# Performance work log

Measured on AMD Instinct MI355X. Metric: run time of the kernel, lower is better.

The kernel has to match this reference:

```python
import jax, jax.numpy as jnp
import numpy as np

NUM_HEADS = 8


def setup_inputs() -> dict:
    key = jax.random.key(0)
    k0, k1, k2 = jax.random.split(key, 3)
    B, C, D, H, W = 2, 256, 16, 16, 8
    x = jax.random.normal(k0, (B, C, D, H, W), dtype=jnp.float32)
    # 1x1x1 Conv3d weights are pointwise linear maps over channels
    w_qkv = jax.random.normal(k1, (3 * C, C), dtype=jnp.float32) * 0.02
    b_qkv = jnp.zeros((3 * C,), dtype=jnp.float32)
    w_out = jax.random.normal(k2, (C, C), dtype=jnp.float32) * 0.02
    b_out = jnp.zeros((C,), dtype=jnp.float32)
    return {"x": x, "w_qkv": w_qkv, "b_qkv": b_qkv, "w_out": w_out, "b_out": b_out}


def reference(x, w_qkv, b_qkv, w_out, b_out):
    b, c, d, h, w = x.shape
    nh = NUM_HEADS
    hd = c // nh
    scale = hd ** (-0.5)
    n = d * h * w
    xf = x.reshape(b, c, n)  # flatten spatial volume to N tokens
    # to_qkv: pointwise conv == channel-mixing matmul
    qkv = jnp.einsum('oc,bcn->bon', w_qkv, xf) + b_qkv[None, :, None]
    # torch: view(b, H, 3*hd, N) then chunk(3, dim=2) -> per-head channel grouping
    qkv = qkv.reshape(b, nh, 3 * hd, n)
    q, k, v = jnp.split(qkv, 3, axis=2)  # each (b, nh, hd, n)
    sim = jnp.einsum('bhcn,bhcm->bhnm', q, k) * scale  # (b, nh, N, N)
    attn = jax.nn.softmax(sim, axis=-1)
    out = jnp.einsum('bhnm,bhcm->bhcn', attn, v)  # (b, nh, hd, N)
    out = out.reshape(b, c, n)
    out = jnp.einsum('oc,bcn->bon', w_out, out) + b_out[None, :, None]
    return x + out.reshape(b, c, d, h, w)
```

## Files before the change

### kernel.cpp

```cpp
#include <hip/hip_runtime.h>
#include <hip/hip_bf16.h>
#include <math.h>

#define BB 2
#define CC 256
#define NH 8
#define HD 32
#define NN 2048
#define KSPAN 1024
#define QBLK 64
#define KTILE 128
#define QK_SCALE 0.25500917f

typedef __attribute__((ext_vector_type(8))) short short8;
typedef __attribute__((ext_vector_type(8))) unsigned short ushort8;
typedef __attribute__((ext_vector_type(4))) float f32x4;

__device__ inline unsigned short f2bf(float f) {
    __hip_bfloat16 h = __float2bfloat16(f);
    return __builtin_bit_cast(unsigned short, h);
}
__device__ inline float bf2f(unsigned short s) {
    unsigned u = (unsigned)s << 16;
    return __builtin_bit_cast(float, u);
}
__device__ inline int kperm(int k) {
    return 32 * (k >> 5) + 16 * ((k >> 2) & 1) + 4 * ((k >> 3) & 3) + (k & 3);
}

__global__ __launch_bounds__(256) void prep(const float* __restrict__ x,
                                            const float* __restrict__ wq,
                                            const float* __restrict__ wo,
                                            unsigned short* __restrict__ xt,
                                            unsigned short* __restrict__ wqb,
                                            unsigned short* __restrict__ wob) {
    const int blk = blockIdx.x, t = threadIdx.x;
    if (blk < 256) {
        const int b = blk >> 7, tile = blk & 127;
        const int c0 = (tile >> 5) * 64, n0 = (tile & 31) * 64;
        __shared__ unsigned short Ts[64][72];
        const float* xb = x + ((size_t)b * CC + c0) * NN + n0;
        const int cl = t >> 4, nl = (t & 15) * 4;
#pragma unroll
        for (int i = 0; i < 4; ++i) {
            float4 v = *(const float4*)&xb[(size_t)(cl + 16 * i) * NN + nl];
            Ts[nl + 0][cl + 16 * i] = f2bf(v.x);
            Ts[nl + 1][cl + 16 * i] = f2bf(v.y);
            Ts[nl + 2][cl + 16 * i] = f2bf(v.z);
            Ts[nl + 3][cl + 16 * i] = f2bf(v.w);
        }
        __syncthreads();
        const int nr = t >> 2, cb = (t & 3) * 16;
        unsigned short* dst = xt + ((size_t)b * NN + n0 + nr) * CC + c0 + cb;
        *(ushort8*)&dst[0] = *(const ushort8*)&Ts[nr][cb];
        *(ushort8*)&dst[8] = *(const ushort8*)&Ts[nr][cb + 8];
    } else if (blk < 264) {
        const int base = (blk - 256) * 24576 + t * 4;
#pragma unroll
        for (int i = 0; i < 24; ++i) {
            int idx = base + i * 1024;
            float4 v = *(const float4*)&wq[idx];
            ushort4 r;
            r.x = f2bf(v.x); r.y = f2bf(v.y); r.z = f2bf(v.z); r.w = f2bf(v.w);
            *(ushort4*)&wqb[idx] = r;
        }
    } else {
        const int base = (blk - 264) * 32768 + t * 4;
#pragma unroll
        for (int i = 0; i < 32; ++i) {
            int idx = base + i * 1024;
            float4 v = *(const float4*)&wo[idx];
            ushort4 r;
            r.x = f2bf(v.x); r.y = f2bf(v.y); r.z = f2bf(v.z); r.w = f2bf(v.w);
            *(ushort4*)&wob[idx] = r;
        }
    }
}

__global__ __launch_bounds__(256) void qkv_mfma(const unsigned short* __restrict__ xt,
                                                const unsigned short* __restrict__ wqb,
                                                const float* __restrict__ bias,
                                                unsigned short* __restrict__ qt,
                                                unsigned short* __restrict__ ktt,
                                                unsigned short* __restrict__ vt) {
    const int b = blockIdx.z, m0 = blockIdx.y * 64, n0 = blockIdx.x * 64;
    const int t = threadIdx.x, lane = t & 63, wid = t >> 6;
    const int g = lane >> 4, ln = lane & 15;
    __shared__ __align__(16) unsigned short Aw[4][64][36];
    __shared__ __align__(16) unsigned short Bx[4][64][36];
    f32x4 acc[4] = {};
    const unsigned short* xb = xt + ((size_t)b * NN + n0) * CC;

    const int sm = t & 63, sch = t >> 6;
    for (int kh = 0; kh < 2; ++kh) {
        __syncthreads();
#pragma unroll
        for (int j = 0; j < 4; ++j) {
            *(ushort8*)&Aw[sch][sm][j * 8] =
                *(const ushort8*)&wqb[(size_t)(m0 + sm) * CC + kh * 128 + sch * 32 + j * 8];
            *(ushort8*)&Bx[sch][sm][j * 8] =
                *(const ushort8*)&xb[(size_t)sm * CC + kh * 128 + sch * 32 + j * 8];
        }
        __syncthreads();
#pragma unroll
        for (int ks = 0; ks < 4; ++ks) {
            short8 aW = *(const short8*)&Aw[ks][wid * 16 + ln][g * 8];
#pragma unroll
            for (int nt = 0; nt < 4; ++nt) {
                short8 bX = *(const short8*)&Bx[ks][nt * 16 + ln][g * 8];
                acc[nt] = __builtin_amdgcn_mfma_f32_16x16x32_bf16(aW, bX, acc[nt], 0, 0, 0);
            }
        }
    }
    const int obase = m0 + wid * 16 + 4 * g;
    const int sect = obase % 96;
    const int type = sect >> 5;
    const int head = obase / 96;
    const int cb4 = obase & 31;
    float bv[4];
#pragma unroll
    for (int r = 0; r < 4; ++r) bv[r] = bias[obase + r];
    if (type == 2) {
#pragma unroll
        for (int nt = 0; nt < 4; ++nt) {
            int n = n0 + nt * 16 + ln;
#pragma unroll
            for (int r = 0; r < 4; ++r)
                vt[((size_t)(b * NH + head) * HD + cb4 + r) * NN + n] = f2bf(acc[nt][r] + bv[r]);
        }
    } else {
        const float sc = (type == 0) ? QK_SCALE : 1.0f;
        unsigned short* dst = (type == 0) ? qt : ktt;
#pragma unroll
        for (int nt = 0; nt < 4; ++nt) {
            int n = n0 + nt * 16 + ln;
            ushort4 r4;
            r4.x = f2bf((acc[nt][0] + bv[0]) * sc);
            r4.y = f2bf((acc[nt][1] + bv[1]) * sc);
            r4.z = f2bf((acc[nt][2] + bv[2]) * sc);
            r4.w = f2bf((acc[nt][3] + bv[3]) * sc);
            *(ushort4*)&dst[((size_t)(b * NH + head) * NN + n) * HD + cb4] = r4;
        }
    }
}

__global__ __launch_bounds__(512) void attn_mfma(const unsigned short* __restrict__ Qt,
                                                 const unsigned short* __restrict__ Kt,
                                                 const unsigned short* __restrict__ Vt,
                                                 unsigned short* __restrict__ aout_t) {
    const int b = blockIdx.z, h = blockIdx.y;
    const int n0 = blockIdx.x * QBLK;
    const int t = threadIdx.x;
    const int lane = t & 63, wid = t >> 6;
    const int g = lane >> 4, ln = lane & 15;
    const int qg = wid & 3, whalf = wid >> 2;

    __shared__ __align__(16) unsigned short Qs[QBLK][40];
    __shared__ __align__(16) unsigned short Ks[2][KTILE][40];
    __shared__ __align__(16) unsigned short Vs[2][HD][136];

    const unsigned short* qb = Qt + ((size_t)(b * NH + h) * NN + n0) * HD;
    const unsigned short* kb = Kt + (size_t)(b * NH + h) * NN * HD;
    const unsigned short* vb = Vt + (size_t)(b * NH + h) * HD * NN;

    if (t < 256) {
        int q = t >> 2, ch = (t & 3) * 8;
        *(ushort8*)&Qs[q][ch] = *(const ushort8*)&qb[(size_t)q * HD + ch];
    }
    __syncthreads();
    const short8 bQ = *(const short8*)&Qs[qg * 16 + ln][g * 8];

    const int th = t & 255, sthalf = t >> 8;
    const int sk = th >> 2, sch = (th & 3) * 8;
    const int row0 = kperm(sk), row1 = kperm(sk + 64);
    const int vcc = th >> 3, vn = (th & 7) * 16;
    const size_t hbase = (size_t)sthalf * KSPAN;

    ushort8 kpre0, kpre1, vpre0, vpre1;
    {
        const unsigned short* ksrc = kb + (hbase + sk) * HD + sch;
        kpre0 = *(const ushort8*)ksrc;
        kpre1 = *(const ushort8*)(ksrc + (size_t)64 * HD);
        const unsigned short* vsrc = vb + (size_t)vcc * NN + hbase + vn;
        vpre0 = *(const ushort8*)vsrc;
        vpre1 = *(const ushort8*)(vsrc + 8);
    }

    float m_run = -1e30f, l_run = 0.f;
    f32x4 oacc[2];
    const f32x4 zero4 = {0.f, 0.f, 0.f, 0.f};
    oacc[0] = zero4; oacc[1] = zero4;

    for (int kt = 0; kt < KSPAN; kt += KTILE) {
        __syncthreads();
        *(ushort8*)&Ks[sthalf][row0][sch] = kpre0;
        *(ushort8*)&Ks[sthalf][row1][sch] = kpre1;
        *(ushort8*)&Vs[sthalf][vcc][vn]     = vpre0;
        *(ushort8*)&Vs[sthalf][vcc][vn + 8] = vpre1;
        __syncthreads();
        if (kt + KTILE < KSPAN) {
            const unsigned short* ksrc = kb + (hbase + kt + KTILE + sk) * HD + sch;
            kpre0 = *(const ushort8*)ksrc;
            kpre1 = *(const ushort8*)(ksrc + (size_t)64 * HD);
            const unsigned short* vsrc = vb + (size_t)vcc * NN + hbase + kt + KTILE + vn;
            vpre0 = *(const ushort8*)vsrc;
            vpre1 = *(const ushort8*)(vsrc + 8);
        }

        f32x4 sacc[8];
        __builtin_amdgcn_s_setprio(1);
#pragma unroll
        for (int t8 = 0; t8 < 8; ++t8) {
            short8 aK = *(const short8*)&Ks[whalf][t8 * 16 + ln][g * 8];
            sacc[t8] = __builtin_amdgcn_mfma_f32_16x16x32_bf16(aK, bQ, zero4, 0, 0, 0);
        }
        __builtin_amdgcn_s_setprio(0);

        float mx[8];
#pragma unroll
        for (int t8 = 0; t8 < 8; ++t8)
            mx[t8] = fmaxf(fmaxf(sacc[t8][0], sacc[t8][1]), fmaxf(sacc[t8][2], sacc[t8][3]));
        float tmax = fmaxf(fmaxf(fmaxf(mx[0], mx[1]), fmaxf(mx[2], mx[3])),
                           fmaxf(fmaxf(mx[4], mx[5]), fmaxf(mx[6], mx[7])));
        tmax = fmaxf(tmax, __shfl_xor(tmax, 16));
        tmax = fmaxf(tmax, __shfl_xor(tmax, 32));
        float mnew = fmaxf(m_run, tmax);
        float rsc = exp2f(m_run - mnew);
#pragma unroll
        for (int t8 = 0; t8 < 8; ++t8) {
            sacc[t8][0] = exp2f(sacc[t8][0] - mnew);
            sacc[t8][1] = exp2f(sacc[t8][1] - mnew);
            sacc[t8][2] = exp2f(sacc[t8][2] - mnew);
            sacc[t8][3] = exp2f(sacc[t8][3] - mnew);
        }
        float ps[8];
#pragma unroll
        for (int t8 = 0; t8 < 8; ++t8)
            ps[t8] = (sacc[t8][0] + sacc[t8][1]) + (sacc[t8][2] + sacc[t8][3]);
        float lsum = ((ps[0] + ps[1]) + (ps[2] + ps[3])) + ((ps[4] + ps[5]) + (ps[6] + ps[7]));
        lsum += __shfl_xor(lsum, 16);
        lsum += __shfl_xor(lsum, 32);
        l_run = l_run * rsc + lsum;
        m_run = mnew;

#pragma unroll
        for (int r = 0; r < 4; ++r) {
            float rr = __shfl(rsc, 4 * g + r);
            oacc[0][r] *= rr;
            oacc[1][r] *= rr;
        }

        short8 aP[4];
#pragma unroll
        for (int kc = 0; kc < 4; ++kc) {
#pragma unroll
            for (int u = 0; u < 2; ++u) {
#pragma unroll
                for (int r = 0; r < 4; ++r)
                    aP[kc][u * 4 + r] = (short)f2bf(sacc[2 * kc + u][r]);
            }
        }

        __builtin_amdgcn_s_setprio(1);
#pragma unroll
        for (int kc = 0; kc < 4; ++kc) {
            short8 bV0 = *(const short8*)&Vs[whalf][ln][kc * 32 + g * 8];
            short8 bV1 = *(const short8*)&Vs[whalf][16 + ln][kc * 32 + g * 8];
            oacc[0] = __builtin_amdgcn_mfma_f32_16x16x32_bf16(aP[kc], bV0, oacc[0], 0, 0, 0);
            oacc[1] = __builtin_amdgcn_mfma_f32_16x16x32_bf16(aP[kc], bV1, oacc[1], 0, 0, 0);
        }
        __builtin_amdgcn_s_setprio(0);
    }

    __syncthreads();
    float*  Of  = (float*)&Ks[0][0][0];
    float2* MLs = (float2*)&Vs[0][0][0];
#pragma unroll
    for (int ct = 0; ct < 2; ++ct)
#pragma unroll
        for (int r = 0; r < 4; ++r)
            Of[((whalf * 64) + qg * 16 + 4 * g + r) * 40 + ct * 16 + ln] = oacc[ct][r];
    if (g == 0) MLs[whalf * 64 + qg * 16 + ln] = make_float2(m_run, l_run);
    __syncthreads();
    {
        const int q = t >> 3, c0 = (t & 7) * 4;
        f32x4 o0 = *(const f32x4*)&Of[(size_t)q * 40 + c0];
        f32x4 o1 = *(const f32x4*)&Of[(size_t)(64 + q) * 40 + c0];
        float2 ml0 = MLs[q], ml1 = MLs[64 + q];
        float M = fmaxf(ml0.x, ml1.x);
        float w0 = exp2f(ml0.x - M), w1 = exp2f(ml1.x - M);
        float dinv = 1.0f / (w0 * ml0.y + w1 * ml1.y);
        w0 *= dinv; w1 *= dinv;
        ushort4 r4;
        r4.x = f2bf(w0 * o0[0] + w1 * o1[0]);
        r4.y = f2bf(w0 * o0[1] + w1 * o1[1]);
        r4.z = f2bf(w0 * o0[2] + w1 * o1[2]);
        r4.w = f2bf(w0 * o0[3] + w1 * o1[3]);
        *(ushort4*)&aout_t[((size_t)b * NN + n0 + q) * CC + h * HD + c0] = r4;
    }
}

__global__ __launch_bounds__(256) void proj_mfma(const unsigned short* __restrict__ aout_t,
                                                 const unsigned short* __restrict__ wob,
                                                 const float* __restrict__ bias,
                                                 const float* __restrict__ x,
                                                 float* __restrict__ out) {
    const int b = blockIdx.z, m0 = blockIdx.y * 64, n0 = blockIdx.x * 32;
    const int t = threadIdx.x, lane = t & 63, wid = t >> 6;
    const int g = lane >> 4, ln = lane & 15;
    __shared__ __align__(16) unsigned short Aw[4][64][36];
    __shared__ __align__(16) unsigned short Bx[4][32][36];
    f32x4 acc[2] = {};
    const unsigned short* ab = aout_t + ((size_t)b * NN + n0) * CC;

    const int sm = t & 63, sch = t >> 6;
    const int bn = t & 31, bch = t >> 5;
    for (int kh = 0; kh < 2; ++kh) {
        __syncthreads();
#pragma unroll
        for (int j = 0; j < 4; ++j)
            *(ushort8*)&Aw[sch][sm][j * 8] =
                *(const ushort8*)&wob[(size_t)(m0 + sm) * CC + kh * 128 + sch * 32 + j * 8];
        {
            int ks = bch >> 1, off = (bch & 1) * 16;
            const unsigned short* src = &ab[(size_t)bn * CC + kh * 128 + ks * 32 + off];
            *(ushort8*)&Bx[ks][bn][off]     = *(const ushort8*)&src[0];
            *(ushort8*)&Bx[ks][bn][off + 8] = *(const ushort8*)&src[8];
        }
        __syncthreads();
#pragma unroll
        for (int ks = 0; ks < 4; ++ks) {
            short8 aW = *(const short8*)&Aw[ks][wid * 16 + ln][g * 8];
#pragma unroll
            for (int nt = 0; nt < 2; ++nt) {
                short8 bX = *(const short8*)&Bx[ks][nt * 16 + ln][g * 8];
                acc[nt] = __builtin_amdgcn_mfma_f32_16x16x32_bf16(aW, bX, acc[nt], 0, 0, 0);
            }
        }
    }
    const int mbase = m0 + wid * 16 + 4 * g;
    float bv[4];
#pragma unroll
    for (int r = 0; r < 4; ++r) bv[r] = bias[mbase + r];
#pragma unroll
    for (int nt = 0; nt < 2; ++nt) {
        int n = n0 + nt * 16 + ln;
#pragma unroll
        for (int r = 0; r < 4; ++r) {
            size_t off = ((size_t)b * CC + mbase + r) * NN + n;
            out[off] = acc[nt][r] + bv[r] + x[off];
        }
    }
}

extern "C" void kernel_launch(void* const* d_in, const int* in_sizes, int n_in,
                              void* d_out, int out_size, void* d_ws, size_t ws_size,
                              hipStream_t stream) {
    const float* x     = (const float*)d_in[0];
    const float* w_qkv = (const float*)d_in[1];
    const float* b_qkv = (const float*)d_in[2];
    const float* w_out = (const float*)d_in[3];
    const float* b_out = (const float*)d_in[4];
    float* out = (float*)d_out;

    unsigned short* xt     = (unsigned short*)d_ws;
    unsigned short* wqb    = xt  + (size_t)BB * NN * CC;
    unsigned short* wob    = wqb + (size_t)768 * CC;
    unsigned short* qt     = wob + (size_t)CC * CC;
    unsigned short* ktt    = qt  + (size_t)BB * NH * NN * HD;
    unsigned short* vt     = ktt + (size_t)BB * NH * NN * HD;
    unsigned short* aout_t = vt  + (size_t)BB * NH * NN * HD;

    prep<<<dim3(266), 256, 0, stream>>>(x, w_qkv, w_out, xt, wqb, wob);
    qkv_mfma<<<dim3(NN / 64, 768 / 64, BB), 256, 0, stream>>>(xt, wqb, b_qkv, qt, ktt, vt);
    attn_mfma<<<dim3(NN / QBLK, NH, BB), 512, 0, stream>>>(qt, ktt, vt, aout_t);
    proj_mfma<<<dim3(NN / 32, CC / 64, BB), 256, 0, stream>>>(aout_t, wob, b_out, x, out);
}
```

Measured before the change: 54.65 us.

## Fuse bf16 conversion into GEMMs and restructure attention with lazy rescale

Removes the separate prep kernel. The QKV and output-projection kernels now load fp32 x and weights directly and convert them to bf16 while staging into shared memory, which saves one launch and a round trip through the workspace. The attention kernel moves to 64-key tiles with double-buffered K/V shared memory and one barrier per iteration. It also skips the online-softmax rescale unless the running max rises by more than a threshold. In exchange, every GEMM block redundantly converts the weights, and the lazy rescale lets exp values grow up to 2^8 before being renormalised.

```diff
diff --git a/kernel.cpp b/kernel.cpp
--- a/kernel.cpp
+++ b/kernel.cpp
@@ -9,7 +9,8 @@
 #define NN 2048
 #define KSPAN 1024
 #define QBLK 64
-#define KTILE 128
+#define KTILE 64
+#define NITER (KSPAN / KTILE)
 #define QK_SCALE 0.25500917f
 
 typedef __attribute__((ext_vector_type(8))) short short8;
@@ -20,65 +21,12 @@
     __hip_bfloat16 h = __float2bfloat16(f);
     return __builtin_bit_cast(unsigned short, h);
 }
-__device__ inline float bf2f(unsigned short s) {
-    unsigned u = (unsigned)s << 16;
-    return __builtin_bit_cast(float, u);
-}
 __device__ inline int kperm(int k) {
     return 32 * (k >> 5) + 16 * ((k >> 2) & 1) + 4 * ((k >> 3) & 3) + (k & 3);
 }
 
-__global__ __launch_bounds__(256) void prep(const float* __restrict__ x,
-                                            const float* __restrict__ wq,
-                                            const float* __restrict__ wo,
-                                            unsigned short* __restrict__ xt,
-                                            unsigned short* __restrict__ wqb,
-                                            unsigned short* __restrict__ wob) {
-    const int blk = blockIdx.x, t = threadIdx.x;
-    if (blk < 256) {
-        const int b = blk >> 7, tile = blk & 127;
-        const int c0 = (tile >> 5) * 64, n0 = (tile & 31) * 64;
-        __shared__ unsigned short Ts[64][72];
-        const float* xb = x + ((size_t)b * CC + c0) * NN + n0;
-        const int cl = t >> 4, nl = (t & 15) * 4;
-#pragma unroll
-        for (int i = 0; i < 4; ++i) {
-            float4 v = *(const float4*)&xb[(size_t)(cl + 16 * i) * NN + nl];
-            Ts[nl + 0][cl + 16 * i] = f2bf(v.x);
-            Ts[nl + 1][cl + 16 * i] = f2bf(v.y);
-            Ts[nl + 2][cl + 16 * i] = f2bf(v.z);
-            Ts[nl + 3][cl + 16 * i] = f2bf(v.w);
-        }
-        __syncthreads();
-        const int nr = t >> 2, cb = (t & 3) * 16;
-        unsigned short* dst = xt + ((size_t)b * NN + n0 + nr) * CC + c0 + cb;
-        *(ushort8*)&dst[0] = *(const ushort8*)&Ts[nr][cb];
-        *(ushort8*)&dst[8] = *(const ushort8*)&Ts[nr][cb + 8];
-    } else if (blk < 264) {
-        const int base = (blk - 256) * 24576 + t * 4;
-#pragma unroll
-        for (int i = 0; i < 24; ++i) {
-            int idx = base + i * 1024;
-            float4 v = *(const float4*)&wq[idx];
-            ushort4 r;
-            r.x = f2bf(v.x); r.y = f2bf(v.y); r.z = f2bf(v.z); r.w = f2bf(v.w);
-            *(ushort4*)&wqb[idx] = r;
-        }
-    } else {
-        const int base = (blk - 264) * 32768 + t * 4;
-#pragma unroll
-        for (int i = 0; i < 32; ++i) {
-            int idx = base + i * 1024;
-            float4 v = *(const float4*)&wo[idx];
-            ushort4 r;
-            r.x = f2bf(v.x); r.y = f2bf(v.y); r.z = f2bf(v.z); r.w = f2bf(v.w);
-            *(ushort4*)&wob[idx] = r;
-        }
-    }
-}
-
-__global__ __launch_bounds__(256) void qkv_mfma(const unsigned short* __restrict__ xt,
-                                                const unsigned short* __restrict__ wqb,
+__global__ __launch_bounds__(256) void qkv_mfma(const float* __restrict__ x,
+                                                const float* __restrict__ wq,
                                                 const float* __restrict__ bias,
                                                 unsigned short* __restrict__ qt,
                                                 unsigned short* __restrict__ ktt,
@@ -89,17 +37,39 @@
     __shared__ __align__(16) unsigned short Aw[4][64][36];
     __shared__ __align__(16) unsigned short Bx[4][64][36];
     f32x4 acc[4] = {};
-    const unsigned short* xb = xt + ((size_t)b * NN + n0) * CC;
 
     const int sm = t & 63, sch = t >> 6;
+    const int pc = t >> 4, pn = t & 15;
+    const int c0 = pc * 8, nl = pn * 4;
+    const float* xb = x + (size_t)b * CC * NN + n0;
+
     for (int kh = 0; kh < 2; ++kh) {
         __syncthreads();
-#pragma unroll
-        for (int j = 0; j < 4; ++j) {
-            *(ushort8*)&Aw[sch][sm][j * 8] =
-                *(const ushort8*)&wqb[(size_t)(m0 + sm) * CC + kh * 128 + sch * 32 + j * 8];
-            *(ushort8*)&Bx[sch][sm][j * 8] =
-                *(const ushort8*)&xb[(size_t)sm * CC + kh * 128 + sch * 32 + j * 8];
+        {
+            const float* wsrc = wq + (size_t)(m0 + sm) * CC + kh * 128 + sch * 32;
+            float wv[32];
+#pragma unroll
+            for (int j = 0; j < 8; ++j) *(float4*)&wv[j * 4] = *(const float4*)&wsrc[j * 4];
+#pragma unroll
+            for (int j2 = 0; j2 < 4; ++j2) {
+                ushort8 p;
+#pragma unroll
+                for (int e = 0; e < 8; ++e) p[e] = f2bf(wv[j2 * 8 + e]);
+                *(ushort8*)&Aw[sch][sm][j2 * 8] = p;
+            }
+        }
+        {
+            const float* xsrc = xb + (size_t)(kh * 128 + c0) * NN + nl;
+            float xv[8][4];
+#pragma unroll
+            for (int i = 0; i < 8; ++i) *(float4*)&xv[i][0] = *(const float4*)&xsrc[(size_t)i * NN];
+#pragma unroll
+            for (int i2 = 0; i2 < 4; ++i2) {
+                ushort8 p;
+#pragma unroll
+                for (int e = 0; e < 8; ++e) p[e] = f2bf(xv[e][i2]);
+                *(ushort8*)&Bx[pc >> 2][nl + i2][(pc & 3) * 8] = p;
+            }
         }
         __syncthreads();
 #pragma unroll
@@ -156,8 +126,8 @@
     const int qg = wid & 3, whalf = wid >> 2;
 
     __shared__ __align__(16) unsigned short Qs[QBLK][40];
-    __shared__ __align__(16) unsigned short Ks[2][KTILE][40];
-    __shared__ __align__(16) unsigned short Vs[2][HD][136];
+    __shared__ __align__(16) unsigned short Ks[2][2][KTILE][40];
+    __shared__ __align__(16) unsigned short Vs[2][2][HD][72];
 
     const unsigned short* qb = Qt + ((size_t)(b * NH + h) * NN + n0) * HD;
     const unsigned short* kb = Kt + (size_t)(b * NH + h) * NN * HD;
@@ -172,100 +142,88 @@
 
     const int th = t & 255, sthalf = t >> 8;
     const int sk = th >> 2, sch = (th & 3) * 8;
-    const int row0 = kperm(sk), row1 = kperm(sk + 64);
-    const int vcc = th >> 3, vn = (th & 7) * 16;
+    const int rowK = kperm(sk);
+    const int vcc = th >> 3, vn = (th & 7) * 8;
     const size_t hbase = (size_t)sthalf * KSPAN;
 
-    ushort8 kpre0, kpre1, vpre0, vpre1;
-    {
-        const unsigned short* ksrc = kb + (hbase + sk) * HD + sch;
-        kpre0 = *(const ushort8*)ksrc;
-        kpre1 = *(const ushort8*)(ksrc + (size_t)64 * HD);
-        const unsigned short* vsrc = vb + (size_t)vcc * NN + hbase + vn;
-        vpre0 = *(const ushort8*)vsrc;
-        vpre1 = *(const ushort8*)(vsrc + 8);
-    }
+    ushort8 kpre, vpre;
+    kpre = *(const ushort8*)&kb[(hbase + sk) * HD + sch];
+    vpre = *(const ushort8*)&vb[(size_t)vcc * NN + hbase + vn];
 
     float m_run = -1e30f, l_run = 0.f;
     f32x4 oacc[2];
     const f32x4 zero4 = {0.f, 0.f, 0.f, 0.f};
     oacc[0] = zero4; oacc[1] = zero4;
 
-    for (int kt = 0; kt < KSPAN; kt += KTILE) {
-        __syncthreads();
-        *(ushort8*)&Ks[sthalf][row0][sch] = kpre0;
-        *(ushort8*)&Ks[sthalf][row1][sch] = kpre1;
-        *(ushort8*)&Vs[sthalf][vcc][vn]     = vpre0;
-        *(ushort8*)&Vs[sthalf][vcc][vn + 8] = vpre1;
-        __syncthreads();
-        if (kt + KTILE < KSPAN) {
-            const unsigned short* ksrc = kb + (hbase + kt + KTILE + sk) * HD + sch;
-            kpre0 = *(const ushort8*)ksrc;
-            kpre1 = *(const ushort8*)(ksrc + (size_t)64 * HD);
-            const unsigned short* vsrc = vb + (size_t)vcc * NN + hbase + kt + KTILE + vn;
-            vpre0 = *(const ushort8*)vsrc;
-            vpre1 = *(const ushort8*)(vsrc + 8);
-        }
-
-        f32x4 sacc[8];
+    for (int it = 0; it < NITER; ++it) {
+        const int buf = it & 1;
+        *(ushort8*)&Ks[sthalf][buf][rowK][sch] = kpre;
+        *(ushort8*)&Vs[sthalf][buf][vcc][vn]   = vpre;
+        if (it + 1 < NITER) {
+            size_t kt = hbase + (size_t)(it + 1) * KTILE;
+            kpre = *(const ushort8*)&kb[(kt + sk) * HD + sch];
+            vpre = *(const ushort8*)&vb[(size_t)vcc * NN + kt + vn];
+        }
+        __syncthreads();
+
+        f32x4 sacc[4];
         __builtin_amdgcn_s_setprio(1);
 #pragma unroll
-        for (int t8 = 0; t8 < 8; ++t8) {
-            short8 aK = *(const short8*)&Ks[whalf][t8 * 16 + ln][g * 8];
+        for (int t8 = 0; t8 < 4; ++t8) {
+            short8 aK = *(const short8*)&Ks[whalf][buf][t8 * 16 + ln][g * 8];
             sacc[t8] = __builtin_amdgcn_mfma_f32_16x16x32_bf16(aK, bQ, zero4, 0, 0, 0);
         }
         __builtin_amdgcn_s_setprio(0);
 
-        float mx[8];
-#pragma unroll
-        for (int t8 = 0; t8 < 8; ++t8)
+        float mx[4];
+#pragma unroll
+        for (int t8 = 0; t8 < 4; ++t8)
             mx[t8] = fmaxf(fmaxf(sacc[t8][0], sacc[t8][1]), fmaxf(sacc[t8][2], sacc[t8][3]));
-        float tmax = fmaxf(fmaxf(fmaxf(mx[0], mx[1]), fmaxf(mx[2], mx[3])),
-                           fmaxf(fmaxf(mx[4], mx[5]), fmaxf(mx[6], mx[7])));
+        float tmax = fmaxf(fmaxf(mx[0], mx[1]), fmaxf(mx[2], mx[3]));
         tmax = fmaxf(tmax, __shfl_xor(tmax, 16));
         tmax = fmaxf(tmax, __shfl_xor(tmax, 32));
-        float mnew = fmaxf(m_run, tmax);
-        float rsc = exp2f(m_run - mnew);
-#pragma unroll
-        for (int t8 = 0; t8 < 8; ++t8) {
-            sacc[t8][0] = exp2f(sacc[t8][0] - mnew);
-            sacc[t8][1] = exp2f(sacc[t8][1] - mnew);
-            sacc[t8][2] = exp2f(sacc[t8][2] - mnew);
-            sacc[t8][3] = exp2f(sacc[t8][3] - mnew);
-        }
-        float ps[8];
-#pragma unroll
-        for (int t8 = 0; t8 < 8; ++t8)
+        if (!__all(tmax <= m_run + 8.0f)) {
+            float mnew = fmaxf(m_run, tmax);
+            float rsc = exp2f(m_run - mnew);
+            m_run = mnew;
+            l_run *= rsc;
+#pragma unroll
+            for (int r = 0; r < 4; ++r) {
+                float rr = __shfl(rsc, 4 * g + r);
+                oacc[0][r] *= rr;
+                oacc[1][r] *= rr;
+            }
+        }
+#pragma unroll
+        for (int t8 = 0; t8 < 4; ++t8) {
+            sacc[t8][0] = exp2f(sacc[t8][0] - m_run);
+            sacc[t8][1] = exp2f(sacc[t8][1] - m_run);
+            sacc[t8][2] = exp2f(sacc[t8][2] - m_run);
+            sacc[t8][3] = exp2f(sacc[t8][3] - m_run);
+        }
+        float ps[4];
+#pragma unroll
+        for (int t8 = 0; t8 < 4; ++t8)
             ps[t8] = (sacc[t8][0] + sacc[t8][1]) + (sacc[t8][2] + sacc[t8][3]);
-        float lsum = ((ps[0] + ps[1]) + (ps[2] + ps[3])) + ((ps[4] + ps[5]) + (ps[6] + ps[7]));
+        float lsum = (ps[0] + ps[1]) + (ps[2] + ps[3]);
         lsum += __shfl_xor(lsum, 16);
         lsum += __shfl_xor(lsum, 32);
-        l_run = l_run * rsc + lsum;
-        m_run = mnew;
-
-#pragma unroll
-        for (int r = 0; r < 4; ++r) {
-            float rr = __shfl(rsc, 4 * g + r);
-            oacc[0][r] *= rr;
-            oacc[1][r] *= rr;
-        }
-
-        short8 aP[4];
-#pragma unroll
-        for (int kc = 0; kc < 4; ++kc) {
-#pragma unroll
-            for (int u = 0; u < 2; ++u) {
+        l_run += lsum;
+
+        short8 aP[2];
+#pragma unroll
+        for (int kc = 0; kc < 2; ++kc)
+#pragma unroll
+            for (int u = 0; u < 2; ++u)
 #pragma unroll
                 for (int r = 0; r < 4; ++r)
                     aP[kc][u * 4 + r] = (short)f2bf(sacc[2 * kc + u][r]);
-            }
-        }
 
         __builtin_amdgcn_s_setprio(1);
 #pragma unroll
-        for (int kc = 0; kc < 4; ++kc) {
-            short8 bV0 = *(const short8*)&Vs[whalf][ln][kc * 32 + g * 8];
-            short8 bV1 = *(const short8*)&Vs[whalf][16 + ln][kc * 32 + g * 8];
+        for (int kc = 0; kc < 2; ++kc) {
+            short8 bV0 = *(const short8*)&Vs[whalf][buf][ln][kc * 32 + g * 8];
+            short8 bV1 = *(const short8*)&Vs[whalf][buf][16 + ln][kc * 32 + g * 8];
             oacc[0] = __builtin_amdgcn_mfma_f32_16x16x32_bf16(aP[kc], bV0, oacc[0], 0, 0, 0);
             oacc[1] = __builtin_amdgcn_mfma_f32_16x16x32_bf16(aP[kc], bV1, oacc[1], 0, 0, 0);
         }
@@ -273,8 +231,8 @@
     }
 
     __syncthreads();
-    float*  Of  = (float*)&Ks[0][0][0];
-    float2* MLs = (float2*)&Vs[0][0][0];
+    float*  Of  = (float*)&Ks[0][0][0][0];
+    float2* MLs = (float2*)&Vs[0][0][0][0];
 #pragma unroll
     for (int ct = 0; ct < 2; ++ct)
 #pragma unroll
@@ -301,7 +259,7 @@
 }
 
 __global__ __launch_bounds__(256) void proj_mfma(const unsigned short* __restrict__ aout_t,
-                                                 const unsigned short* __restrict__ wob,
+                                                 const float* __restrict__ wo,
                                                  const float* __restrict__ bias,
                                                  const float* __restrict__ x,
                                                  float* __restrict__ out) {
@@ -317,10 +275,19 @@
     const int bn = t & 31, bch = t >> 5;
     for (int kh = 0; kh < 2; ++kh) {
         __syncthreads();
-#pragma unroll
-        for (int j = 0; j < 4; ++j)
-            *(ushort8*)&Aw[sch][sm][j * 8] =
-                *(const ushort8*)&wob[(size_t)(m0 + sm) * CC + kh * 128 + sch * 32 + j * 8];
+        {
+            const float* wsrc = wo + (size_t)(m0 + sm) * CC + kh * 128 + sch * 32;
+            float wv[32];
+#pragma unroll
+            for (int j = 0; j < 8; ++j) *(float4*)&wv[j * 4] = *(const float4*)&wsrc[j * 4];
+#pragma unroll
+            for (int j2 = 0; j2 < 4; ++j2) {
+                ushort8 p;
+#pragma unroll
+                for (int e = 0; e < 8; ++e) p[e] = f2bf(wv[j2 * 8 + e]);
+                *(ushort8*)&Aw[sch][sm][j2 * 8] = p;
+            }
+        }
         {
             int ks = bch >> 1, off = (bch & 1) * 16;
             const unsigned short* src = &ab[(size_t)bn * CC + kh * 128 + ks * 32 + off];
@@ -363,16 +330,12 @@
     const float* b_out = (const float*)d_in[4];
     float* out = (float*)d_out;
 
-    unsigned short* xt     = (unsigned short*)d_ws;
-    unsigned short* wqb    = xt  + (size_t)BB * NN * CC;
-    unsigned short* wob    = wqb + (size_t)768 * CC;
-    unsigned short* qt     = wob + (size_t)CC * CC;
+    unsigned short* qt     = (unsigned short*)d_ws;
     unsigned short* ktt    = qt  + (size_t)BB * NH * NN * HD;
     unsigned short* vt     = ktt + (size_t)BB * NH * NN * HD;
     unsigned short* aout_t = vt  + (size_t)BB * NH * NN * HD;
 
-    prep<<<dim3(266), 256, 0, stream>>>(x, w_qkv, w_out, xt, wqb, wob);
-    qkv_mfma<<<dim3(NN / 64, 768 / 64, BB), 256, 0, stream>>>(xt, wqb, b_qkv, qt, ktt, vt);
+    qkv_mfma<<<dim3(NN / 64, 768 / 64, BB), 256, 0, stream>>>(x, w_qkv, b_qkv, qt, ktt, vt);
     attn_mfma<<<dim3(NN / QBLK, NH, BB), 512, 0, stream>>>(qt, ktt, vt, aout_t);
-    proj_mfma<<<dim3(NN / 32, CC / 64, BB), 256, 0, stream>>>(aout_t, wob, b_out, x, out);
-}
+    proj_mfma<<<dim3(NN / 32, CC / 64, BB), 256, 0, stream>>>(aout_t, w_out, b_out, x, out);
+}
```

Measured after the change: 53.52 us. 2.1% less time.
